# Kernel optimization log

Measured on AMD Instinct MI355X. Metric: run time of the kernel, lower is better.

The kernel has to match this reference:

```python
import jax, jax.numpy as jnp
import numpy as np

N_NODES = 50000
N_EDGES = 800000
HID = 128
N_PROC = 3  # num_layers - 1 processor iterations (shared weights)


def _mlp(x, w1, b1, w2, b2, w3, b3):
    h = jax.nn.relu(x @ w1 + b1)
    h = jax.nn.relu(h @ w2 + b2)
    return h @ w3 + b3


def setup_inputs() -> dict:
    key = jax.random.key(0)
    ks = jax.random.split(key, 32)

    def p(k, shape):
        fan_in = shape[0]
        return (jax.random.normal(k, shape, dtype=jnp.float32) / np.float32(np.sqrt(fan_in)))

    inp = {
        "X_curr": jax.random.normal(ks[0], (N_NODES, 6), dtype=jnp.float32),
        "y_prev": jax.random.normal(ks[1], (N_NODES,), dtype=jnp.float32),
        "edge": jax.random.randint(ks[2], (2, N_EDGES), 0, N_NODES, dtype=jnp.int32),
        "mode": 0,
        # EdgeModel net: Linear(9,H) ReLU Linear(H,H) ReLU Linear(H,3)
        "ew1": p(ks[3], (9, HID)), "eb1": jnp.zeros((HID,), jnp.float32),
        "ew2": p(ks[4], (HID, HID)), "eb2": jnp.zeros((HID,), jnp.float32),
        "ew3": p(ks[5], (HID, 3)), "eb3": jnp.zeros((3,), jnp.float32),
        # NodeModel net: Linear(5,H) ReLU Linear(H,H) ReLU Linear(H,1)
        "nw1": p(ks[6], (5, HID)), "nb1": jnp.zeros((HID,), jnp.float32),
        "nw2": p(ks[7], (HID, HID)), "nb2": jnp.zeros((HID,), jnp.float32),
        "nw3": p(ks[8], (HID, 1)), "nb3": jnp.zeros((1,), jnp.float32),
        # decoder: Linear(5,H) ReLU Linear(H,H) ReLU Linear(H,H) ReLU Linear(H,1)
        "dw1": p(ks[9], (5, HID)), "db1": jnp.zeros((HID,), jnp.float32),
        "dw2": p(ks[10], (HID, HID)), "db2": jnp.zeros((HID,), jnp.float32),
        "dw3": p(ks[11], (HID, HID)), "db3": jnp.zeros((HID,), jnp.float32),
        "dw4": p(ks[12], (HID, 1)), "db4": jnp.zeros((1,), jnp.float32),
    }
    return inp


def reference(X_curr, y_prev,
              ew1, eb1, ew2, eb2, ew3, eb3,
              nw1, nb1, nw2, nb2, nw3, nb3,
              dw1, db1, dw2, db2, dw3, db3, dw4, db4,
              edge, mode):
    n = X_curr.shape[0]
    src_idx, dst_idx = edge[0], edge[1]
    # x_in = cat(X_curr[:, [0,1,2,4]], y_prev)  -> [N, 5]
    x = jnp.concatenate([X_curr[:, jnp.array([0, 1, 2, 4])], y_prev[:, None]], axis=-1)

    # _compute_edge_attr: grad_r = (f_dest - f_src) * disp_r
    xs, xd = x[src_idx], x[dst_idx]
    disp = xd[:, :3] - xs[:, :3]
    edge_attr = (xd[:, 4] - xs[:, 4])[:, None] * disp  # [E, 3]

    # degree for scatter-mean (nodes with no incoming edges aggregate to 0)
    deg = jax.ops.segment_sum(jnp.ones((edge.shape[1],), x.dtype), dst_idx, num_segments=n)
    inv_deg = jnp.where(deg > 0, 1.0 / jnp.maximum(deg, 1.0), 0.0)

    for _ in range(N_PROC):
        # EdgeModel
        xs, xd = x[src_idx], x[dst_idx]
        disp = xd[:, :3] - xs[:, :3]
        norm_r = jnp.linalg.norm(disp, axis=-1, keepdims=True)
        net_in = jnp.concatenate([disp, norm_r, edge_attr, xs[:, 4:5], xd[:, 4:5]], axis=-1)  # [E, 9]
        edge_attr = edge_attr + _mlp(net_in, ew1, eb1, ew2, eb2, ew3, eb3)
        # NodeModel: message = edge_attr, aggr='mean' at target (edge[1])
        aggr = jax.ops.segment_sum(edge_attr, dst_idx, num_segments=n) * inv_deg[:, None]  # [N, 3]
        node_in = jnp.concatenate([x[:, 3:5], aggr], axis=-1)  # [N, 5]
        delta = _mlp(node_in, nw1, nb1, nw2, nb2, nw3, nb3)[:, 0]
        x = x.at[:, 4].add(delta)

    # decoder
    h = jax.nn.relu(x @ dw1 + db1)
    h = jax.nn.relu(h @ dw2 + db2)
    h = jax.nn.relu(h @ dw3 + db3)
    x_out = h @ dw4 + db4  # [N, 1]
    return y_prev + x_out[:, 0]
```

## Files before the change

kernel.cpp:

```cpp
#include <hip/hip_runtime.h>

typedef float f32x4 __attribute__((ext_vector_type(4)));
typedef __bf16 bf16x8 __attribute__((ext_vector_type(8)));
typedef __bf16 bf16x4 __attribute__((ext_vector_type(4)));

#define WB_W1E 0
#define WB_W2E 4096
#define WB_W3E 20480
#define WB_W1N 22528
#define WB_W2N 26624
#define WB_W3N 43008
#define WB_W1D 45056
#define WB_W2D 49152
#define WB_W3D 65536
#define WB_W4D 81920
#define WB_TOTAL 83968

#define BKT_SHIFT 6
#define BKT_SZ 64

__global__ void k_prep(const float* __restrict__ ew1, const float* __restrict__ eb1,
                       const float* __restrict__ ew2, const float* __restrict__ ew3,
                       const float* __restrict__ nw1, const float* __restrict__ nb1,
                       const float* __restrict__ nw2, const float* __restrict__ nw3,
                       const float* __restrict__ dw1, const float* __restrict__ db1,
                       const float* __restrict__ dw2, const float* __restrict__ dw3,
                       const float* __restrict__ dw4, __bf16* __restrict__ wb) {
  int gid = blockIdx.x * 256 + threadIdx.x;
  if (gid >= WB_TOTAL) return;
  const float* srcs[10] = {ew1, ew2, ew3, nw1, nw2, nw3, dw1, dw2, dw3, dw4};
  const float* brow[10] = {eb1, 0, 0, nb1, 0, 0, db1, 0, 0, 0};
  const int Ks[10] = {9, 128, 128, 5, 128, 128, 5, 128, 128, 128};
  const int Ns[10] = {128, 128, 3, 128, 128, 1, 128, 128, 128, 1};
  const int CTs[10] = {8, 8, 1, 8, 8, 1, 8, 8, 8, 1};
  const int cum[11] = {0, 4096, 20480, 22528, 26624, 43008, 45056, 49152, 65536, 81920, 83968};
  int seg = 0;
  while (gid >= cum[seg + 1]) seg++;
  int li = gid - cum[seg];
  int j = li & 7;
  int lane = (li >> 3) & 63;
  int fi = li >> 9;
  int CT = CTs[seg];
  int ct = fi % CT;
  int kt = fi / CT;
  int k = kt * 32 + ((lane >> 4) << 3) + j;
  int n = ct * 16 + (lane & 15);
  int kl;
  if (seg == 0) {
    if (k < 4) kl = k;
    else if (k >= 8 && k < 13) kl = k - 4;
    else kl = (k == 13) ? -2 : -1;
  } else if (seg == 3 || seg == 6) {
    if (k < 5) kl = k;
    else kl = (k == 5) ? -2 : -1;
  } else {
    kl = (k < Ks[seg]) ? k : -1;
  }
  float v = 0.f;
  if (n < Ns[seg]) {
    if (kl >= 0) v = srcs[seg][kl * Ns[seg] + n];
    else if (kl == -2 && brow[seg]) v = brow[seg][n];
  }
  wb[gid] = (__bf16)v;
}

__global__ void k_zero(const float* __restrict__ y_prev, float* __restrict__ x4,
                       int* __restrict__ cnt, int n) {
  int i = blockIdx.x * 256 + threadIdx.x;
  if (i < n) {
    x4[i] = y_prev[i];
    cnt[i] = 0;
  }
}

__global__ void k_count(const int* __restrict__ dstp, int* __restrict__ cnt, int E) {
  int e = blockIdx.x * 256 + threadIdx.x;
  if (e < E) atomicAdd(cnt + dstp[e], 1);
}

__global__ void k_scan_block(const int* __restrict__ cnt, int* __restrict__ rp,
                             float* __restrict__ invdeg, int* __restrict__ bsum, int n) {
  __shared__ int sd[256];
  int t = threadIdx.x;
  int i = blockIdx.x * 256 + t;
  int c = (i < n) ? cnt[i] : 0;
  if (i < n) invdeg[i] = c > 0 ? 1.0f / (float)c : 0.f;
  sd[t] = c;
  __syncthreads();
#pragma unroll
  for (int off = 1; off < 256; off <<= 1) {
    int v = sd[t];
    int u = (t >= off) ? sd[t - off] : 0;
    __syncthreads();
    sd[t] = v + u;
    __syncthreads();
  }
  if (i < n) rp[i] = sd[t] - c;
  if (t == 255) bsum[blockIdx.x] = sd[255];
}

__global__ void k_scan_top(int* __restrict__ bsum, int nb) {
  __shared__ int sd[1024];
  int t = threadIdx.x;
  int c = (t < nb) ? bsum[t] : 0;
  sd[t] = c;
  __syncthreads();
#pragma unroll
  for (int off = 1; off < 1024; off <<= 1) {
    int v = sd[t];
    int u = (t >= off) ? sd[t - off] : 0;
    __syncthreads();
    sd[t] = v + u;
    __syncthreads();
  }
  if (t < nb) bsum[t] = sd[t] - c;
}

__global__ void k_scan_add(int* __restrict__ rp, const int* __restrict__ bsum,
                           int* __restrict__ cur, int n, int E) {
  int i = blockIdx.x * 256 + threadIdx.x;
  if (i < n) {
    int v = rp[i] + bsum[blockIdx.x];
    rp[i] = v;
    if ((i & (BKT_SZ - 1)) == 0) cur[i >> BKT_SHIFT] = v;
  }
  if (i == 0) rp[n] = E;
}

__global__ __launch_bounds__(256) void k_bin(const int* __restrict__ dstp, int* __restrict__ cur,
                                             int* __restrict__ eix, int nbkt, int E) {
  __shared__ int hist[1024];
  __shared__ int base[1024];
  int tid = threadIdx.x;
  for (int t = tid; t < nbkt; t += 256) hist[t] = 0;
  __syncthreads();
  int e0 = blockIdx.x * 8192;
  int b[32], lr[32];
#pragma unroll
  for (int j = 0; j < 32; j++) {
    int e = e0 + j * 256 + tid;
    if (e < E) {
      b[j] = dstp[e] >> BKT_SHIFT;
      lr[j] = atomicAdd(&hist[b[j]], 1);
    } else {
      b[j] = -1;
      lr[j] = 0;
    }
  }
  __syncthreads();
  for (int t = tid; t < nbkt; t += 256) {
    int c = hist[t];
    base[t] = c ? atomicAdd(&cur[t], c) : 0;
  }
  __syncthreads();
#pragma unroll
  for (int j = 0; j < 32; j++)
    if (b[j] >= 0) eix[base[b[j]] + lr[j]] = e0 + j * 256 + tid;
}

__global__ __launch_bounds__(256) void k_build(const int* __restrict__ srcO,
                                               const int* __restrict__ dstO,
                                               const float* __restrict__ Xc,
                                               const float* __restrict__ yp,
                                               const int* __restrict__ rp, const int* eix,
                                               int* __restrict__ srcS, int* dstS,
                                               float* __restrict__ peS, float* __restrict__ eaS,
                                               int n) {
  __shared__ int rpl[BKT_SZ + 1];
  __shared__ int cnt[BKT_SZ];
  int tid = threadIdx.x;
  int d0 = blockIdx.x << BKT_SHIFT;
  if (tid <= BKT_SZ) {
    int d = d0 + tid;
    if (d > n) d = n;
    rpl[tid] = rp[d];
  }
  if (tid < BKT_SZ) cnt[tid] = 0;
  __syncthreads();
  int dlim = n - d0;
  if (dlim > BKT_SZ) dlim = BKT_SZ;
  int gstart = rpl[0], gend = rpl[dlim];
  int ei[16];
#pragma unroll
  for (int k = 0; k < 16; k++) {
    int p = gstart + k * 256 + tid;
    ei[k] = (p < gend) ? eix[p] : -1;
  }
  __syncthreads();
#pragma unroll
  for (int k = 0; k < 16; k++) {
    int e = ei[k];
    if (e < 0) continue;
    int s = srcO[e], d = dstO[e];
    float dx = Xc[d * 6 + 0] - Xc[s * 6 + 0];
    float dy = Xc[d * 6 + 1] - Xc[s * 6 + 1];
    float dz = Xc[d * 6 + 2] - Xc[s * 6 + 2];
    float nr = sqrtf(dx * dx + dy * dy + dz * dz);
    float w = yp[d] - yp[s];
    int r = atomicAdd(&cnt[d - d0], 1);
    int q = rpl[d - d0] + r;
    srcS[q] = s;
    dstS[q] = d;
    f32x4 pv = {dx, dy, dz, nr};
    *(f32x4*)(peS + 4 * q) = pv;
    f32x4 av = {w * dx, w * dy, w * dz, 0.f};
    *(f32x4*)(eaS + 4 * q) = av;
  }
}

__device__ __forceinline__ int aoff(int row, int b) { return (row * 256 + b) ^ ((row & 7) << 4); }

__device__ __forceinline__ void wg_sync() {
  asm volatile("s_waitcnt lgkmcnt(0)" ::: "memory");
  __builtin_amdgcn_s_barrier();
}

__device__ __forceinline__ bf16x4 relu_pack(f32x4 a) {
  bf16x4 p;
#pragma unroll
  for (int r = 0; r < 4; r++) {
    float v = a[r];
    p[r] = (__bf16)(v > 0.f ? v : 0.f);
  }
  return p;
}

__global__ __attribute__((amdgpu_flat_work_group_size(256, 256), amdgpu_waves_per_eu(2, 8))) void
k_edge(const float* __restrict__ x4, const float* __restrict__ pe, float* __restrict__ ea,
       const int* __restrict__ src, const int* __restrict__ dstp,
       const __bf16* __restrict__ W1f, const __bf16* __restrict__ W2f,
       const __bf16* __restrict__ W3f, const float* __restrict__ b2,
       const float* __restrict__ b3, int ntiles, int E) {
  __shared__ char Ab[16384];
  __shared__ char Bb[16384];
  const int tid = threadIdx.x;
  const int l = tid & 63, w = tid >> 6;
  const int col = l & 15, krow = l >> 4;
  const int rl = w * 16 + (l >> 2), chunk = l & 3;

  bf16x8 w1r[2], w2r[4][2], w3r[4];
#pragma unroll
  for (int t = 0; t < 2; t++) w1r[t] = *(const bf16x8*)(W1f + ((2 * w + t) << 9) + l * 8);
#pragma unroll
  for (int kt = 0; kt < 4; kt++)
#pragma unroll
    for (int t = 0; t < 2; t++)
      w2r[kt][t] = *(const bf16x8*)(W2f + ((kt * 8 + 2 * w + t) << 9) + l * 8);
#pragma unroll
  for (int kt = 0; kt < 4; kt++) w3r[kt] = *(const bf16x8*)(W3f + (kt << 9) + l * 8);
  f32x4 b2c[2];
#pragma unroll
  for (int t = 0; t < 2; t++) b2c[t] = *(const f32x4*)(b2 + (2 * w + t) * 16 + krow * 4);
  f32x4 b3i = {0.f, 0.f, 0.f, 0.f};
  if (krow == 0) {
    b3i[0] = b3[0];
    b3i[1] = b3[1];
    b3i[2] = b3[2];
  }

  int tile = blockIdx.x;
  if (tile >= ntiles) return;

  int e0 = tile * 64 + rl;
  int ec = e0 < E ? e0 : E - 1;
  int cs = src[ec], cd = dstp[ec];
  f32x4 cld = {0.f, 0.f, 0.f, 0.f};
  if (chunk < 2) cld = *(const f32x4*)(((chunk == 1) ? ea : pe) + 4 * ec);
  float cxs = 0.f, cxd = 0.f;
  if (chunk == 1) {
    cxs = x4[cs];
    cxd = x4[cd];
  }

  for (;;) {
    bf16x8 v;
#pragma unroll
    for (int q = 0; q < 8; q++) v[q] = (__bf16)0.f;
    if (chunk == 0) {
      v[0] = (__bf16)cld[0];
      v[1] = (__bf16)cld[1];
      v[2] = (__bf16)cld[2];
      v[3] = (__bf16)cld[3];
    } else if (chunk == 1) {
      v[0] = (__bf16)cld[0];
      v[1] = (__bf16)cld[1];
      v[2] = (__bf16)cld[2];
      v[3] = (__bf16)cxs;
      v[4] = (__bf16)cxd;
      v[5] = (__bf16)1.0f;
    }
    *(bf16x8*)(Ab + aoff(rl, chunk * 16)) = v;

    int nt = tile + (int)gridDim.x;
    bool hn = nt < ntiles;
    int tc = hn ? nt : tile;
    int en = tc * 64 + rl;
    if (en >= E) en = E - 1;
    int ns = src[en], nd = dstp[en];

    wg_sync();

    f32x4 h[4][2];
#pragma unroll
    for (int c = 0; c < 4; c++)
#pragma unroll
      for (int t = 0; t < 2; t++) {
        f32x4 z = {0.f, 0.f, 0.f, 0.f};
        h[c][t] = z;
      }
    bf16x8 bb[4];
#pragma unroll
    for (int c = 0; c < 4; c++) bb[c] = *(const bf16x8*)(Ab + aoff(c * 16 + col, krow * 16));
#pragma unroll
    for (int c = 0; c < 4; c++)
#pragma unroll
      for (int t = 0; t < 2; t++)
        h[c][t] = __builtin_amdgcn_mfma_f32_16x16x32_bf16(w1r[t], bb[c], h[c][t], 0, 0, 0);
#pragma unroll
    for (int c = 0; c < 4; c++)
#pragma unroll
      for (int t = 0; t < 2; t++)
        *(bf16x4*)(Bb + aoff(c * 16 + col, (2 * w + t) * 32 + krow * 8)) = relu_pack(h[c][t]);

    wg_sync();

    f32x4 nld = {0.f, 0.f, 0.f, 0.f};
    if (chunk < 2) nld = *(const f32x4*)(((chunk == 1) ? ea : pe) + 4 * en);
    float nxs = 0.f, nxd = 0.f;
    if (chunk == 1) {
      nxs = x4[ns];
      nxd = x4[nd];
    }

#pragma unroll
    for (int c = 0; c < 4; c++)
#pragma unroll
      for (int t = 0; t < 2; t++) h[c][t] = b2c[t];
#pragma unroll
    for (int kt = 0; kt < 4; kt++) {
#pragma unroll
      for (int c = 0; c < 4; c++)
        bb[c] = *(const bf16x8*)(Bb + aoff(c * 16 + col, kt * 64 + krow * 16));
#pragma unroll
      for (int c = 0; c < 4; c++)
#pragma unroll
        for (int t = 0; t < 2; t++)
          h[c][t] = __builtin_amdgcn_mfma_f32_16x16x32_bf16(w2r[kt][t], bb[c], h[c][t], 0, 0, 0);
    }
#pragma unroll
    for (int c = 0; c < 4; c++)
#pragma unroll
      for (int t = 0; t < 2; t++)
        *(bf16x4*)(Ab + aoff(c * 16 + col, (2 * w + t) * 32 + krow * 8)) = relu_pack(h[c][t]);

    wg_sync();

    f32x4 o = b3i;
#pragma unroll
    for (int kt = 0; kt < 4; kt++) {
      bf16x8 bq = *(const bf16x8*)(Ab + aoff(w * 16 + col, kt * 64 + krow * 16));
      o = __builtin_amdgcn_mfma_f32_16x16x32_bf16(w3r[kt], bq, o, 0, 0, 0);
    }

    if (krow == 0) {
      int e3 = tile * 64 + w * 16 + col;
      if (e3 < E) {
        f32x4 oe = *(const f32x4*)(ea + 4 * e3);
        f32x4 nv;
        nv[0] = oe[0] + o[0];
        nv[1] = oe[1] + o[1];
        nv[2] = oe[2] + o[2];
        nv[3] = 0.f;
        *(f32x4*)(ea + 4 * e3) = nv;
      }
    }

    if (!hn) break;
    tile = nt;
    cld = nld;
    cxs = nxs;
    cxd = nxd;
  }
}

__global__ __attribute__((amdgpu_flat_work_group_size(256, 256), amdgpu_waves_per_eu(3, 4))) void
k_node(float* __restrict__ x4, const float* __restrict__ Xc, const float* __restrict__ eaS,
       const int* __restrict__ rp, const float* __restrict__ invdeg,
       const __bf16* __restrict__ W1f, const __bf16* __restrict__ W2f,
       const __bf16* __restrict__ W3f, const float* __restrict__ b2,
       const float* __restrict__ b3, int n) {
  __shared__ char Ab[16384];
  __shared__ char Bb[16384];
  const int tid = threadIdx.x;
  const int l = tid & 63, w = tid >> 6;
  const int col = l & 15, krow = l >> 4;
  const int rl = w * 16 + (l >> 2), chunk = l & 3;

  bf16x8 w1r[2], w2r[4][2], w3r[4];
#pragma unroll
  for (int t = 0; t < 2; t++) w1r[t] = *(const bf16x8*)(W1f + ((2 * w + t) << 9) + l * 8);
#pragma unroll
  for (int kt = 0; kt < 4; kt++)
#pragma unroll
    for (int t = 0; t < 2; t++)
      w2r[kt][t] = *(const bf16x8*)(W2f + ((kt * 8 + 2 * w + t) << 9) + l * 8);
#pragma unroll
  for (int kt = 0; kt < 4; kt++) w3r[kt] = *(const bf16x8*)(W3f + (kt << 9) + l * 8);
  f32x4 b2c[2];
#pragma unroll
  for (int t = 0; t < 2; t++) b2c[t] = *(const f32x4*)(b2 + (2 * w + t) * 16 + krow * 4);
  float b3s = b3[0];

  int tile = blockIdx.x;
  int i0 = tile * 64 + rl;
  bool vi = i0 < n;
  int i = vi ? i0 : (n - 1);

  int ss = rp[i], se = rp[i + 1];
  float a0 = 0.f, a1 = 0.f, a2 = 0.f;
  for (int p = ss + chunk; p < se; p += 4) {
    f32x4 ev = *(const f32x4*)(eaS + 4 * p);
    a0 += ev[0];
    a1 += ev[1];
    a2 += ev[2];
  }
  a0 += __shfl_xor(a0, 1);
  a1 += __shfl_xor(a1, 1);
  a2 += __shfl_xor(a2, 1);
  a0 += __shfl_xor(a0, 2);
  a1 += __shfl_xor(a1, 2);
  a2 += __shfl_xor(a2, 2);

  bf16x8 v;
#pragma unroll
  for (int q = 0; q < 8; q++) v[q] = (__bf16)0.f;
  if (chunk == 0) {
    float x3 = Xc[i * 6 + 4];
    float xv = x4[i];
    float iv = invdeg[i];
    v[0] = (__bf16)x3;
    v[1] = (__bf16)xv;
    v[2] = (__bf16)(a0 * iv);
    v[3] = (__bf16)(a1 * iv);
    v[4] = (__bf16)(a2 * iv);
    v[5] = (__bf16)1.0f;
  }
  *(bf16x8*)(Ab + aoff(rl, chunk * 16)) = v;

  wg_sync();

  f32x4 h[4][2];
#pragma unroll
  for (int c = 0; c < 4; c++)
#pragma unroll
    for (int t = 0; t < 2; t++) {
      f32x4 z = {0.f, 0.f, 0.f, 0.f};
      h[c][t] = z;
    }
  bf16x8 bb[4];
#pragma unroll
  for (int c = 0; c < 4; c++) bb[c] = *(const bf16x8*)(Ab + aoff(c * 16 + col, krow * 16));
#pragma unroll
  for (int c = 0; c < 4; c++)
#pragma unroll
    for (int t = 0; t < 2; t++)
      h[c][t] = __builtin_amdgcn_mfma_f32_16x16x32_bf16(w1r[t], bb[c], h[c][t], 0, 0, 0);
#pragma unroll
  for (int c = 0; c < 4; c++)
#pragma unroll
    for (int t = 0; t < 2; t++)
      *(bf16x4*)(Bb + aoff(c * 16 + col, (2 * w + t) * 32 + krow * 8)) = relu_pack(h[c][t]);

  wg_sync();

#pragma unroll
  for (int c = 0; c < 4; c++)
#pragma unroll
    for (int t = 0; t < 2; t++) h[c][t] = b2c[t];
#pragma unroll
  for (int kt = 0; kt < 4; kt++) {
#pragma unroll
    for (int c = 0; c < 4; c++)
      bb[c] = *(const bf16x8*)(Bb + aoff(c * 16 + col, kt * 64 + krow * 16));
#pragma unroll
    for (int c = 0; c < 4; c++)
#pragma unroll
      for (int t = 0; t < 2; t++)
        h[c][t] = __builtin_amdgcn_mfma_f32_16x16x32_bf16(w2r[kt][t], bb[c], h[c][t], 0, 0, 0);
  }
#pragma unroll
  for (int c = 0; c < 4; c++)
#pragma unroll
    for (int t = 0; t < 2; t++)
      *(bf16x4*)(Ab + aoff(c * 16 + col, (2 * w + t) * 32 + krow * 8)) = relu_pack(h[c][t]);

  wg_sync();

  f32x4 o = {0.f, 0.f, 0.f, 0.f};
  if (krow == 0) o[0] = b3s;
#pragma unroll
  for (int kt = 0; kt < 4; kt++) {
    bf16x8 bq = *(const bf16x8*)(Ab + aoff(w * 16 + col, kt * 64 + krow * 16));
    o = __builtin_amdgcn_mfma_f32_16x16x32_bf16(w3r[kt], bq, o, 0, 0, 0);
  }

  if (krow == 0) {
    int i3 = tile * 64 + w * 16 + col;
    if (i3 < n) x4[i3] = x4[i3] + o[0];
  }
}

__global__ __attribute__((amdgpu_flat_work_group_size(256, 256), amdgpu_waves_per_eu(2, 4))) void
k_dec(const float* __restrict__ x4, const float* __restrict__ Xc, const float* __restrict__ y_prev,
      const __bf16* __restrict__ W1f, const __bf16* __restrict__ W2f,
      const __bf16* __restrict__ W3f, const __bf16* __restrict__ W4f,
      const float* __restrict__ b2, const float* __restrict__ b3, const float* __restrict__ b4,
      float* __restrict__ out, int n) {
  __shared__ char Ab[16384];
  __shared__ char Bb[16384];
  const int tid = threadIdx.x;
  const int l = tid & 63, w = tid >> 6;
  const int col = l & 15, krow = l >> 4;
  const int rl = w * 16 + (l >> 2), chunk = l & 3;

  bf16x8 w1r[2], w2r[4][2], w3r[4][2], w4r[4];
#pragma unroll
  for (int t = 0; t < 2; t++) w1r[t] = *(const bf16x8*)(W1f + ((2 * w + t) << 9) + l * 8);
#pragma unroll
  for (int kt = 0; kt < 4; kt++)
#pragma unroll
    for (int t = 0; t < 2; t++) {
      w2r[kt][t] = *(const bf16x8*)(W2f + ((kt * 8 + 2 * w + t) << 9) + l * 8);
      w3r[kt][t] = *(const bf16x8*)(W3f + ((kt * 8 + 2 * w + t) << 9) + l * 8);
    }
#pragma unroll
  for (int kt = 0; kt < 4; kt++) w4r[kt] = *(const bf16x8*)(W4f + (kt << 9) + l * 8);
  f32x4 b2c[2], b3c[2];
#pragma unroll
  for (int t = 0; t < 2; t++) {
    b2c[t] = *(const f32x4*)(b2 + (2 * w + t) * 16 + krow * 4);
    b3c[t] = *(const f32x4*)(b3 + (2 * w + t) * 16 + krow * 4);
  }
  float b4s = b4[0];

  int tile = blockIdx.x;
  int i0 = tile * 64 + rl;
  bool vi = i0 < n;
  int i = vi ? i0 : (n - 1);

  bf16x8 v;
#pragma unroll
  for (int q = 0; q < 8; q++) v[q] = (__bf16)0.f;
  if (chunk == 0) {
    v[0] = (__bf16)Xc[i * 6 + 0];
    v[1] = (__bf16)Xc[i * 6 + 1];
    v[2] = (__bf16)Xc[i * 6 + 2];
    v[3] = (__bf16)Xc[i * 6 + 4];
    v[4] = (__bf16)x4[i];
    v[5] = (__bf16)1.0f;
  }
  *(bf16x8*)(Ab + aoff(rl, chunk * 16)) = v;

  wg_sync();

  f32x4 h[4][2];
  bf16x8 bb[4];
#pragma unroll
  for (int c = 0; c < 4; c++)
#pragma unroll
    for (int t = 0; t < 2; t++) {
      f32x4 z = {0.f, 0.f, 0.f, 0.f};
      h[c][t] = z;
    }
#pragma unroll
  for (int c = 0; c < 4; c++) bb[c] = *(const bf16x8*)(Ab + aoff(c * 16 + col, krow * 16));
#pragma unroll
  for (int c = 0; c < 4; c++)
#pragma unroll
    for (int t = 0; t < 2; t++)
      h[c][t] = __builtin_amdgcn_mfma_f32_16x16x32_bf16(w1r[t], bb[c], h[c][t], 0, 0, 0);
#pragma unroll
  for (int c = 0; c < 4; c++)
#pragma unroll
    for (int t = 0; t < 2; t++)
      *(bf16x4*)(Bb + aoff(c * 16 + col, (2 * w + t) * 32 + krow * 8)) = relu_pack(h[c][t]);

  wg_sync();

#pragma unroll
  for (int c = 0; c < 4; c++)
#pragma unroll
    for (int t = 0; t < 2; t++) h[c][t] = b2c[t];
#pragma unroll
  for (int kt = 0; kt < 4; kt++) {
#pragma unroll
    for (int c = 0; c < 4; c++)
      bb[c] = *(const bf16x8*)(Bb + aoff(c * 16 + col, kt * 64 + krow * 16));
#pragma unroll
    for (int c = 0; c < 4; c++)
#pragma unroll
      for (int t = 0; t < 2; t++)
        h[c][t] = __builtin_amdgcn_mfma_f32_16x16x32_bf16(w2r[kt][t], bb[c], h[c][t], 0, 0, 0);
  }
#pragma unroll
  for (int c = 0; c < 4; c++)
#pragma unroll
    for (int t = 0; t < 2; t++)
      *(bf16x4*)(Ab + aoff(c * 16 + col, (2 * w + t) * 32 + krow * 8)) = relu_pack(h[c][t]);

  wg_sync();

#pragma unroll
  for (int c = 0; c < 4; c++)
#pragma unroll
    for (int t = 0; t < 2; t++) h[c][t] = b3c[t];
#pragma unroll
  for (int kt = 0; kt < 4; kt++) {
#pragma unroll
    for (int c = 0; c < 4; c++)
      bb[c] = *(const bf16x8*)(Ab + aoff(c * 16 + col, kt * 64 + krow * 16));
#pragma unroll
    for (int c = 0; c < 4; c++)
#pragma unroll
      for (int t = 0; t < 2; t++)
        h[c][t] = __builtin_amdgcn_mfma_f32_16x16x32_bf16(w3r[kt][t], bb[c], h[c][t], 0, 0, 0);
  }
#pragma unroll
  for (int c = 0; c < 4; c++)
#pragma unroll
    for (int t = 0; t < 2; t++)
      *(bf16x4*)(Bb + aoff(c * 16 + col, (2 * w + t) * 32 + krow * 8)) = relu_pack(h[c][t]);

  wg_sync();

  f32x4 o = {0.f, 0.f, 0.f, 0.f};
  if (krow == 0) o[0] = b4s;
#pragma unroll
  for (int kt = 0; kt < 4; kt++) {
    bf16x8 bq = *(const bf16x8*)(Bb + aoff(w * 16 + col, kt * 64 + krow * 16));
    o = __builtin_amdgcn_mfma_f32_16x16x32_bf16(w4r[kt], bq, o, 0, 0, 0);
  }

  if (krow == 0) {
    int i3 = tile * 64 + w * 16 + col;
    if (i3 < n) out[i3] = y_prev[i3] + o[0];
  }
}

extern "C" void kernel_launch(void* const* d_in, const int* in_sizes, int n_in, void* d_out,
                              int out_size, void* d_ws, size_t ws_size, hipStream_t stream) {
  const float* Xc = (const float*)d_in[0];
  const float* y_prev = (const float*)d_in[1];
  const int* edge = (const int*)d_in[2];
  const float* ew1 = (const float*)d_in[4];
  const float* eb1 = (const float*)d_in[5];
  const float* ew2 = (const float*)d_in[6];
  const float* eb2 = (const float*)d_in[7];
  const float* ew3 = (const float*)d_in[8];
  const float* eb3 = (const float*)d_in[9];
  const float* nw1 = (const float*)d_in[10];
  const float* nb1 = (const float*)d_in[11];
  const float* nw2 = (const float*)d_in[12];
  const float* nb2 = (const float*)d_in[13];
  const float* nw3 = (const float*)d_in[14];
  const float* nb3 = (const float*)d_in[15];
  const float* dw1 = (const float*)d_in[16];
  const float* db1 = (const float*)d_in[17];
  const float* dw2 = (const float*)d_in[18];
  const float* db2 = (const float*)d_in[19];
  const float* dw3 = (const float*)d_in[20];
  const float* db3 = (const float*)d_in[21];
  const float* dw4 = (const float*)d_in[22];
  const float* db4 = (const float*)d_in[23];

  int n = in_sizes[0] / 6;
  int E = in_sizes[2] / 2;
  const int* srcp = edge;
  const int* dstp = edge + E;

  __bf16* wb = (__bf16*)d_ws;
  float* fbase = (float*)((char*)d_ws + (size_t)WB_TOTAL * 2);
  size_t na = ((size_t)n + 3) & ~(size_t)3;
  float* x4 = fbase;
  float* invdeg = fbase + na;
  int* cnt = (int*)(fbase + 2 * na);
  int* rp = cnt + na;
  int* bsum = rp + na + 8;
  int* cur = bsum + 1024;
  int* srcS = cur + 1024;
  int* dstS = srcS + E;
  float* peS = (float*)(dstS + E);
  float* eaS = peS + 4 * (size_t)E;

  size_t need = (size_t)WB_TOTAL * 2 + (4 * na + 8 + 2048 + 10 * (size_t)E) * 4;
  if (ws_size < need) return;

  dim3 B(256);
  int nblk = (n + 255) / 256;
  int nbkt = (n + BKT_SZ - 1) / BKT_SZ;
  k_prep<<<dim3((WB_TOTAL + 255) / 256), B, 0, stream>>>(ew1, eb1, ew2, ew3, nw1, nb1, nw2, nw3,
                                                         dw1, db1, dw2, dw3, dw4, wb);
  k_zero<<<dim3(nblk), B, 0, stream>>>(y_prev, x4, cnt, n);
  k_count<<<dim3((E + 255) / 256), B, 0, stream>>>(dstp, cnt, E);
  k_scan_block<<<dim3(nblk), B, 0, stream>>>(cnt, rp, invdeg, bsum, n);
  k_scan_top<<<dim3(1), dim3(1024), 0, stream>>>(bsum, nblk);
  k_scan_add<<<dim3(nblk), B, 0, stream>>>(rp, bsum, cur, n, E);
  k_bin<<<dim3((E + 8191) / 8192), B, 0, stream>>>(dstp, cur, dstS, nbkt, E);
  k_build<<<dim3(nbkt), B, 0, stream>>>(srcp, dstp, Xc, y_prev, rp, dstS, srcS, dstS, peS, eaS, n);

  int etiles = (E + 63) / 64;
  int vtiles = (n + 63) / 64;
  int egrid = etiles < 2048 ? etiles : 2048;
  for (int it = 0; it < 3; it++) {
    k_edge<<<dim3(egrid), B, 0, stream>>>(x4, peS, eaS, srcS, dstS, wb + WB_W1E, wb + WB_W2E,
                                          wb + WB_W3E, eb2, eb3, etiles, E);
    k_node<<<dim3(vtiles), B, 0, stream>>>(x4, Xc, eaS, rp, invdeg, wb + WB_W1N, wb + WB_W2N,
                                           wb + WB_W3N, nb2, nb3, n);
  }
  k_dec<<<dim3(vtiles), B, 0, stream>>>(x4, Xc, y_prev, wb + WB_W1D, wb + WB_W2D, wb + WB_W3D,
                                        wb + WB_W4D, db2, db3, db4, (float*)d_out, n);
}
```

Before: 296.8 us.

## Split edge MLP across eight waves per block with one output-column tile each

The edge kernel moves from 256 to 512 threads per block, so each of the eight waves owns one 16-column slice of the hidden layers instead of two. This halves per-wave weight registers and accumulators, aiming for higher occupancy and more latency hiding. Only half of each wave stages inputs, and only four waves run the final layer. An extra barrier at the end of each tile iteration guards LDS reuse, and the persistent grid is halved. The cost is more barrier traffic and idle lanes during staging and the last layer.

```diff
diff --git a/kernel.cpp b/kernel.cpp
--- a/kernel.cpp
+++ b/kernel.cpp
@@ -225,7 +225,7 @@
   return p;
 }
 
-__global__ __attribute__((amdgpu_flat_work_group_size(256, 256), amdgpu_waves_per_eu(2, 8))) void
+__global__ __attribute__((amdgpu_flat_work_group_size(512, 512), amdgpu_waves_per_eu(4, 8))) void
 k_edge(const float* __restrict__ x4, const float* __restrict__ pe, float* __restrict__ ea,
        const int* __restrict__ src, const int* __restrict__ dstp,
        const __bf16* __restrict__ W1f, const __bf16* __restrict__ W2f,
@@ -236,23 +236,20 @@
   const int tid = threadIdx.x;
   const int l = tid & 63, w = tid >> 6;
   const int col = l & 15, krow = l >> 4;
-  const int rl = w * 16 + (l >> 2), chunk = l & 3;
-
-  bf16x8 w1r[2], w2r[4][2], w3r[4];
-#pragma unroll
-  for (int t = 0; t < 2; t++) w1r[t] = *(const bf16x8*)(W1f + ((2 * w + t) << 9) + l * 8);
+  const int rl = w * 8 + (l >> 2), chunk = l & 3;
+  const bool stager = l < 32;
+
+  bf16x8 w1r = *(const bf16x8*)(W1f + (w << 9) + l * 8);
+  bf16x8 w2r[4];
 #pragma unroll
   for (int kt = 0; kt < 4; kt++)
-#pragma unroll
-    for (int t = 0; t < 2; t++)
-      w2r[kt][t] = *(const bf16x8*)(W2f + ((kt * 8 + 2 * w + t) << 9) + l * 8);
+    w2r[kt] = *(const bf16x8*)(W2f + ((kt * 8 + w) << 9) + l * 8);
+  bf16x8 w3r[4];
 #pragma unroll
   for (int kt = 0; kt < 4; kt++) w3r[kt] = *(const bf16x8*)(W3f + (kt << 9) + l * 8);
-  f32x4 b2c[2];
-#pragma unroll
-  for (int t = 0; t < 2; t++) b2c[t] = *(const f32x4*)(b2 + (2 * w + t) * 16 + krow * 4);
+  f32x4 b2c = *(const f32x4*)(b2 + w * 16 + krow * 4);
   f32x4 b3i = {0.f, 0.f, 0.f, 0.f};
-  if (krow == 0) {
+  if (w < 4 && krow == 0) {
     b3i[0] = b3[0];
     b3i[1] = b3[1];
     b3i[2] = b3[2];
@@ -263,79 +260,79 @@
 
   int e0 = tile * 64 + rl;
   int ec = e0 < E ? e0 : E - 1;
-  int cs = src[ec], cd = dstp[ec];
   f32x4 cld = {0.f, 0.f, 0.f, 0.f};
-  if (chunk < 2) cld = *(const f32x4*)(((chunk == 1) ? ea : pe) + 4 * ec);
   float cxs = 0.f, cxd = 0.f;
-  if (chunk == 1) {
-    cxs = x4[cs];
-    cxd = x4[cd];
+  if (stager) {
+    if (chunk < 2) cld = *(const f32x4*)(((chunk == 1) ? ea : pe) + 4 * ec);
+    if (chunk == 1) {
+      cxs = x4[src[ec]];
+      cxd = x4[dstp[ec]];
+    }
   }
 
   for (;;) {
-    bf16x8 v;
-#pragma unroll
-    for (int q = 0; q < 8; q++) v[q] = (__bf16)0.f;
-    if (chunk == 0) {
-      v[0] = (__bf16)cld[0];
-      v[1] = (__bf16)cld[1];
-      v[2] = (__bf16)cld[2];
-      v[3] = (__bf16)cld[3];
-    } else if (chunk == 1) {
-      v[0] = (__bf16)cld[0];
-      v[1] = (__bf16)cld[1];
-      v[2] = (__bf16)cld[2];
-      v[3] = (__bf16)cxs;
-      v[4] = (__bf16)cxd;
-      v[5] = (__bf16)1.0f;
-    }
-    *(bf16x8*)(Ab + aoff(rl, chunk * 16)) = v;
+    if (stager) {
+      bf16x8 v;
+#pragma unroll
+      for (int q = 0; q < 8; q++) v[q] = (__bf16)0.f;
+      if (chunk == 0) {
+        v[0] = (__bf16)cld[0];
+        v[1] = (__bf16)cld[1];
+        v[2] = (__bf16)cld[2];
+        v[3] = (__bf16)cld[3];
+      } else if (chunk == 1) {
+        v[0] = (__bf16)cld[0];
+        v[1] = (__bf16)cld[1];
+        v[2] = (__bf16)cld[2];
+        v[3] = (__bf16)cxs;
+        v[4] = (__bf16)cxd;
+        v[5] = (__bf16)1.0f;
+      }
+      *(bf16x8*)(Ab + aoff(rl, chunk * 16)) = v;
+    }
 
     int nt = tile + (int)gridDim.x;
     bool hn = nt < ntiles;
     int tc = hn ? nt : tile;
     int en = tc * 64 + rl;
     if (en >= E) en = E - 1;
-    int ns = src[en], nd = dstp[en];
+    int ns = 0, nd = 0;
+    if (stager && chunk == 1) {
+      ns = src[en];
+      nd = dstp[en];
+    }
 
     wg_sync();
 
-    f32x4 h[4][2];
-#pragma unroll
-    for (int c = 0; c < 4; c++)
-#pragma unroll
-      for (int t = 0; t < 2; t++) {
-        f32x4 z = {0.f, 0.f, 0.f, 0.f};
-        h[c][t] = z;
+    f32x4 h[4];
+    bf16x8 bb[4];
+#pragma unroll
+    for (int c = 0; c < 4; c++) {
+      f32x4 z = {0.f, 0.f, 0.f, 0.f};
+      h[c] = z;
+      bb[c] = *(const bf16x8*)(Ab + aoff(c * 16 + col, krow * 16));
+    }
+#pragma unroll
+    for (int c = 0; c < 4; c++)
+      h[c] = __builtin_amdgcn_mfma_f32_16x16x32_bf16(w1r, bb[c], h[c], 0, 0, 0);
+#pragma unroll
+    for (int c = 0; c < 4; c++)
+      *(bf16x4*)(Bb + aoff(c * 16 + col, w * 32 + krow * 8)) = relu_pack(h[c]);
+
+    wg_sync();
+
+    f32x4 nld = {0.f, 0.f, 0.f, 0.f};
+    float nxs = 0.f, nxd = 0.f;
+    if (stager) {
+      if (chunk < 2) nld = *(const f32x4*)(((chunk == 1) ? ea : pe) + 4 * en);
+      if (chunk == 1) {
+        nxs = x4[ns];
+        nxd = x4[nd];
       }
-    bf16x8 bb[4];
-#pragma unroll
-    for (int c = 0; c < 4; c++) bb[c] = *(const bf16x8*)(Ab + aoff(c * 16 + col, krow * 16));
-#pragma unroll
-    for (int c = 0; c < 4; c++)
-#pragma unroll
-      for (int t = 0; t < 2; t++)
-        h[c][t] = __builtin_amdgcn_mfma_f32_16x16x32_bf16(w1r[t], bb[c], h[c][t], 0, 0, 0);
-#pragma unroll
-    for (int c = 0; c < 4; c++)
-#pragma unroll
-      for (int t = 0; t < 2; t++)
-        *(bf16x4*)(Bb + aoff(c * 16 + col, (2 * w + t) * 32 + krow * 8)) = relu_pack(h[c][t]);
-
-    wg_sync();
-
-    f32x4 nld = {0.f, 0.f, 0.f, 0.f};
-    if (chunk < 2) nld = *(const f32x4*)(((chunk == 1) ? ea : pe) + 4 * en);
-    float nxs = 0.f, nxd = 0.f;
-    if (chunk == 1) {
-      nxs = x4[ns];
-      nxd = x4[nd];
-    }
-
-#pragma unroll
-    for (int c = 0; c < 4; c++)
-#pragma unroll
-      for (int t = 0; t < 2; t++) h[c][t] = b2c[t];
+    }
+
+#pragma unroll
+    for (int c = 0; c < 4; c++) h[c] = b2c;
 #pragma unroll
     for (int kt = 0; kt < 4; kt++) {
 #pragma unroll
@@ -343,35 +340,32 @@
         bb[c] = *(const bf16x8*)(Bb + aoff(c * 16 + col, kt * 64 + krow * 16));
 #pragma unroll
       for (int c = 0; c < 4; c++)
-#pragma unroll
-        for (int t = 0; t < 2; t++)
-          h[c][t] = __builtin_amdgcn_mfma_f32_16x16x32_bf16(w2r[kt][t], bb[c], h[c][t], 0, 0, 0);
-    }
-#pragma unroll
-    for (int c = 0; c < 4; c++)
-#pragma unroll
-      for (int t = 0; t < 2; t++)
-        *(bf16x4*)(Ab + aoff(c * 16 + col, (2 * w + t) * 32 + krow * 8)) = relu_pack(h[c][t]);
+        h[c] = __builtin_amdgcn_mfma_f32_16x16x32_bf16(w2r[kt], bb[c], h[c], 0, 0, 0);
+    }
+#pragma unroll
+    for (int c = 0; c < 4; c++)
+      *(bf16x4*)(Ab + aoff(c * 16 + col, w * 32 + krow * 8)) = relu_pack(h[c]);
 
     wg_sync();
 
-    f32x4 o = b3i;
-#pragma unroll
-    for (int kt = 0; kt < 4; kt++) {
-      bf16x8 bq = *(const bf16x8*)(Ab + aoff(w * 16 + col, kt * 64 + krow * 16));
-      o = __builtin_amdgcn_mfma_f32_16x16x32_bf16(w3r[kt], bq, o, 0, 0, 0);
-    }
-
-    if (krow == 0) {
-      int e3 = tile * 64 + w * 16 + col;
-      if (e3 < E) {
-        f32x4 oe = *(const f32x4*)(ea + 4 * e3);
-        f32x4 nv;
-        nv[0] = oe[0] + o[0];
-        nv[1] = oe[1] + o[1];
-        nv[2] = oe[2] + o[2];
-        nv[3] = 0.f;
-        *(f32x4*)(ea + 4 * e3) = nv;
+    if (w < 4) {
+      f32x4 o = b3i;
+#pragma unroll
+      for (int kt = 0; kt < 4; kt++) {
+        bf16x8 bq = *(const bf16x8*)(Ab + aoff(w * 16 + col, kt * 64 + krow * 16));
+        o = __builtin_amdgcn_mfma_f32_16x16x32_bf16(w3r[kt], bq, o, 0, 0, 0);
+      }
+      if (krow == 0) {
+        int e3 = tile * 64 + w * 16 + col;
+        if (e3 < E) {
+          f32x4 oe = *(const f32x4*)(ea + 4 * e3);
+          f32x4 nv;
+          nv[0] = oe[0] + o[0];
+          nv[1] = oe[1] + o[1];
+          nv[2] = oe[2] + o[2];
+          nv[3] = 0.f;
+          *(f32x4*)(ea + 4 * e3) = nv;
+        }
       }
     }
 
@@ -380,6 +374,7 @@
     cld = nld;
     cxs = nxs;
     cxd = nxd;
+    wg_sync();
   }
 }
 
@@ -710,10 +705,10 @@
 
   int etiles = (E + 63) / 64;
   int vtiles = (n + 63) / 64;
-  int egrid = etiles < 2048 ? etiles : 2048;
+  int egrid = etiles < 1024 ? etiles : 1024;
   for (int it = 0; it < 3; it++) {
-    k_edge<<<dim3(egrid), B, 0, stream>>>(x4, peS, eaS, srcS, dstS, wb + WB_W1E, wb + WB_W2E,
-                                          wb + WB_W3E, eb2, eb3, etiles, E);
+    k_edge<<<dim3(egrid), dim3(512), 0, stream>>>(x4, peS, eaS, srcS, dstS, wb + WB_W1E,
+                                                  wb + WB_W2E, wb + WB_W3E, eb2, eb3, etiles, E);
     k_node<<<dim3(vtiles), B, 0, stream>>>(x4, Xc, eaS, rp, invdeg, wb + WB_W1N, wb + WB_W2N,
                                            wb + WB_W3N, nb2, nb3, n);
   }
```

After: 346.1 us. 16.6% more time.

## Build CSR from bucket-level histogram and retune edge kernel occupancy and grid

Applied to the files above, without the earlier changes.

Replaces the per-node atomic count plus three-kernel scan with a shared-memory bucket histogram and a single-block scan over buckets. Per-node row pointers and inverse degrees are now computed inside the build kernel with a wavefront prefix scan over local counts. Separately, the edge MLP kernel gets a waves-per-EU hint of 3 to 4 and its persistent grid is capped at 768 blocks instead of 2048. This cuts launches and global atomics in preprocessing, but the occupancy and grid change could hurt load balance in the edge kernel.

```diff
diff --git a/kernel.cpp b/kernel.cpp
--- a/kernel.cpp
+++ b/kernel.cpp
@@ -65,44 +65,36 @@
 }
 
 __global__ void k_zero(const float* __restrict__ y_prev, float* __restrict__ x4,
-                       int* __restrict__ cnt, int n) {
+                       int* __restrict__ bcnt, int n, int nbkt) {
   int i = blockIdx.x * 256 + threadIdx.x;
-  if (i < n) {
-    x4[i] = y_prev[i];
-    cnt[i] = 0;
-  }
-}
-
-__global__ void k_count(const int* __restrict__ dstp, int* __restrict__ cnt, int E) {
-  int e = blockIdx.x * 256 + threadIdx.x;
-  if (e < E) atomicAdd(cnt + dstp[e], 1);
-}
-
-__global__ void k_scan_block(const int* __restrict__ cnt, int* __restrict__ rp,
-                             float* __restrict__ invdeg, int* __restrict__ bsum, int n) {
-  __shared__ int sd[256];
-  int t = threadIdx.x;
-  int i = blockIdx.x * 256 + t;
-  int c = (i < n) ? cnt[i] : 0;
-  if (i < n) invdeg[i] = c > 0 ? 1.0f / (float)c : 0.f;
-  sd[t] = c;
-  __syncthreads();
-#pragma unroll
-  for (int off = 1; off < 256; off <<= 1) {
-    int v = sd[t];
-    int u = (t >= off) ? sd[t - off] : 0;
-    __syncthreads();
-    sd[t] = v + u;
-    __syncthreads();
-  }
-  if (i < n) rp[i] = sd[t] - c;
-  if (t == 255) bsum[blockIdx.x] = sd[255];
-}
-
-__global__ void k_scan_top(int* __restrict__ bsum, int nb) {
+  if (i < n) x4[i] = y_prev[i];
+  if (i <= nbkt) bcnt[i] = 0;
+}
+
+__global__ __launch_bounds__(256) void k_cntb(const int* __restrict__ dstp,
+                                              int* __restrict__ bcnt, int nbkt, int E) {
+  __shared__ int hist[1024];
+  int tid = threadIdx.x;
+  for (int t = tid; t < nbkt; t += 256) hist[t] = 0;
+  __syncthreads();
+  int e0 = blockIdx.x * 8192;
+#pragma unroll
+  for (int j = 0; j < 32; j++) {
+    int e = e0 + j * 256 + tid;
+    if (e < E) atomicAdd(&hist[dstp[e] >> BKT_SHIFT], 1);
+  }
+  __syncthreads();
+  for (int t = tid; t < nbkt; t += 256) {
+    int c = hist[t];
+    if (c) atomicAdd(&bcnt[t], c);
+  }
+}
+
+__global__ void k_scanb(const int* __restrict__ bcnt, int* __restrict__ bstart,
+                        int* __restrict__ cur, int* __restrict__ rp, int nbkt, int n, int E) {
   __shared__ int sd[1024];
   int t = threadIdx.x;
-  int c = (t < nb) ? bsum[t] : 0;
+  int c = (t < nbkt) ? bcnt[t] : 0;
   sd[t] = c;
   __syncthreads();
 #pragma unroll
@@ -113,18 +105,15 @@
     sd[t] = v + u;
     __syncthreads();
   }
-  if (t < nb) bsum[t] = sd[t] - c;
-}
-
-__global__ void k_scan_add(int* __restrict__ rp, const int* __restrict__ bsum,
-                           int* __restrict__ cur, int n, int E) {
-  int i = blockIdx.x * 256 + threadIdx.x;
-  if (i < n) {
-    int v = rp[i] + bsum[blockIdx.x];
-    rp[i] = v;
-    if ((i & (BKT_SZ - 1)) == 0) cur[i >> BKT_SHIFT] = v;
-  }
-  if (i == 0) rp[n] = E;
+  if (t < nbkt) {
+    int ex = sd[t] - c;
+    bstart[t] = ex;
+    cur[t] = ex;
+  }
+  if (t == 0) {
+    bstart[nbkt] = E;
+    rp[n] = E;
+  }
 }
 
 __global__ __launch_bounds__(256) void k_bin(const int* __restrict__ dstp, int* __restrict__ cur,
@@ -162,43 +151,60 @@
                                                const int* __restrict__ dstO,
                                                const float* __restrict__ Xc,
                                                const float* __restrict__ yp,
-                                               const int* __restrict__ rp, const int* eix,
+                                               const int* __restrict__ bstart, const int* eix,
                                                int* __restrict__ srcS, int* dstS,
                                                float* __restrict__ peS, float* __restrict__ eaS,
+                                               int* __restrict__ rp, float* __restrict__ invdeg,
                                                int n) {
-  __shared__ int rpl[BKT_SZ + 1];
   __shared__ int cnt[BKT_SZ];
+  __shared__ int starts[BKT_SZ];
   int tid = threadIdx.x;
   int d0 = blockIdx.x << BKT_SHIFT;
-  if (tid <= BKT_SZ) {
-    int d = d0 + tid;
-    if (d > n) d = n;
-    rpl[tid] = rp[d];
-  }
   if (tid < BKT_SZ) cnt[tid] = 0;
-  __syncthreads();
-  int dlim = n - d0;
-  if (dlim > BKT_SZ) dlim = BKT_SZ;
-  int gstart = rpl[0], gend = rpl[dlim];
-  int ei[16];
+  int gstart = bstart[blockIdx.x], gend = bstart[blockIdx.x + 1];
+  __syncthreads();
+  int ei[16], dd[16], rr[16];
 #pragma unroll
   for (int k = 0; k < 16; k++) {
     int p = gstart + k * 256 + tid;
     ei[k] = (p < gend) ? eix[p] : -1;
   }
+#pragma unroll
+  for (int k = 0; k < 16; k++) {
+    if (ei[k] >= 0) {
+      dd[k] = dstO[ei[k]];
+      rr[k] = atomicAdd(&cnt[dd[k] - d0], 1);
+    }
+  }
+  __syncthreads();
+  if (tid < 64) {
+    int c = cnt[tid];
+    int s = c;
+#pragma unroll
+    for (int off = 1; off < 64; off <<= 1) {
+      int u = __shfl_up(s, off);
+      if (tid >= off) s += u;
+    }
+    int ex = s - c;
+    starts[tid] = ex;
+    int d = d0 + tid;
+    if (d < n) {
+      rp[d] = gstart + ex;
+      invdeg[d] = c > 0 ? 1.0f / (float)c : 0.f;
+    }
+  }
   __syncthreads();
 #pragma unroll
   for (int k = 0; k < 16; k++) {
     int e = ei[k];
     if (e < 0) continue;
-    int s = srcO[e], d = dstO[e];
+    int s = srcO[e], d = dd[k];
     float dx = Xc[d * 6 + 0] - Xc[s * 6 + 0];
     float dy = Xc[d * 6 + 1] - Xc[s * 6 + 1];
     float dz = Xc[d * 6 + 2] - Xc[s * 6 + 2];
     float nr = sqrtf(dx * dx + dy * dy + dz * dz);
     float w = yp[d] - yp[s];
-    int r = atomicAdd(&cnt[d - d0], 1);
-    int q = rpl[d - d0] + r;
+    int q = gstart + starts[d - d0] + rr[k];
     srcS[q] = s;
     dstS[q] = d;
     f32x4 pv = {dx, dy, dz, nr};
@@ -225,7 +231,7 @@
   return p;
 }
 
-__global__ __attribute__((amdgpu_flat_work_group_size(256, 256), amdgpu_waves_per_eu(2, 8))) void
+__global__ __attribute__((amdgpu_flat_work_group_size(256, 256), amdgpu_waves_per_eu(3, 4))) void
 k_edge(const float* __restrict__ x4, const float* __restrict__ pe, float* __restrict__ ea,
        const int* __restrict__ src, const int* __restrict__ dstp,
        const __bf16* __restrict__ W1f, const __bf16* __restrict__ W2f,
@@ -683,34 +689,34 @@
   size_t na = ((size_t)n + 3) & ~(size_t)3;
   float* x4 = fbase;
   float* invdeg = fbase + na;
-  int* cnt = (int*)(fbase + 2 * na);
-  int* rp = cnt + na;
-  int* bsum = rp + na + 8;
-  int* cur = bsum + 1024;
+  int* rp = (int*)(fbase + 2 * na);
+  int* bcnt = rp + na + 8;
+  int* bstart = bcnt + 1056;
+  int* cur = bstart + 1056;
   int* srcS = cur + 1024;
   int* dstS = srcS + E;
   float* peS = (float*)(dstS + E);
   float* eaS = peS + 4 * (size_t)E;
 
-  size_t need = (size_t)WB_TOTAL * 2 + (4 * na + 8 + 2048 + 10 * (size_t)E) * 4;
+  size_t need = (size_t)WB_TOTAL * 2 + (3 * na + 8 + 3136 + 10 * (size_t)E) * 4;
   if (ws_size < need) return;
 
   dim3 B(256);
   int nblk = (n + 255) / 256;
   int nbkt = (n + BKT_SZ - 1) / BKT_SZ;
+  int eblk = (E + 8191) / 8192;
   k_prep<<<dim3((WB_TOTAL + 255) / 256), B, 0, stream>>>(ew1, eb1, ew2, ew3, nw1, nb1, nw2, nw3,
                                                          dw1, db1, dw2, dw3, dw4, wb);
-  k_zero<<<dim3(nblk), B, 0, stream>>>(y_prev, x4, cnt, n);
-  k_count<<<dim3((E + 255) / 256), B, 0, stream>>>(dstp, cnt, E);
-  k_scan_block<<<dim3(nblk), B, 0, stream>>>(cnt, rp, invdeg, bsum, n);
-  k_scan_top<<<dim3(1), dim3(1024), 0, stream>>>(bsum, nblk);
-  k_scan_add<<<dim3(nblk), B, 0, stream>>>(rp, bsum, cur, n, E);
-  k_bin<<<dim3((E + 8191) / 8192), B, 0, stream>>>(dstp, cur, dstS, nbkt, E);
-  k_build<<<dim3(nbkt), B, 0, stream>>>(srcp, dstp, Xc, y_prev, rp, dstS, srcS, dstS, peS, eaS, n);
+  k_zero<<<dim3(nblk), B, 0, stream>>>(y_prev, x4, bcnt, n, nbkt);
+  k_cntb<<<dim3(eblk), B, 0, stream>>>(dstp, bcnt, nbkt, E);
+  k_scanb<<<dim3(1), dim3(1024), 0, stream>>>(bcnt, bstart, cur, rp, nbkt, n, E);
+  k_bin<<<dim3(eblk), B, 0, stream>>>(dstp, cur, dstS, nbkt, E);
+  k_build<<<dim3(nbkt), B, 0, stream>>>(srcp, dstp, Xc, y_prev, bstart, dstS, srcS, dstS, peS,
+                                        eaS, rp, invdeg, n);
 
   int etiles = (E + 63) / 64;
   int vtiles = (n + 63) / 64;
-  int egrid = etiles < 2048 ? etiles : 2048;
+  int egrid = etiles < 768 ? etiles : 768;
   for (int it = 0; it < 3; it++) {
     k_edge<<<dim3(egrid), B, 0, stream>>>(x4, peS, eaS, srcS, dstS, wb + WB_W1E, wb + WB_W2E,
                                           wb + WB_W3E, eb2, eb3, etiles, E);
```

Result: faster. 253.6 us (-14.6%).
